# Kernel optimization log

Hardware: AMD Instinct MI355X
Metric: run time of the kernel (lower is better)

Reference implementation:

```python
import jax, jax.numpy as jnp
import numpy as np

B, M, D, H, FF = 2, 2048, 1024, 16, 2624
DH = D // H  # 64, power of 2 as required by the kernel
EPS = 1e-5
THETA = 10000.0


def setup_inputs() -> dict:
    key = jax.random.key(0)
    ks = jax.random.split(key, 12)
    hidden_states = jax.random.normal(ks[0], (B, M, D), dtype=jnp.float32)
    # padding mask: 1=valid, 0=pad; vary valid lengths per batch element
    lengths = jnp.array([M, 3 * M // 4], dtype=jnp.int32)
    attention_mask = (jnp.arange(M)[None, :] < lengths[:, None]).astype(jnp.int32)
    s = 0.02
    return {
        "hidden_states": hidden_states,
        "attention_mask": attention_mask,
        "ln1_w": jnp.ones((D,), jnp.float32),
        "ln1_b": jnp.zeros((D,), jnp.float32),
        "wqkv_w": s * jax.random.normal(ks[1], (3 * D, D), jnp.float32),
        "wqkv_b": jnp.zeros((3 * D,), jnp.float32),
        "wo_w": s * jax.random.normal(ks[2], (D, D), jnp.float32),
        "ln2_w": jnp.ones((D,), jnp.float32),
        "ln2_b": jnp.zeros((D,), jnp.float32),
        "wi_w": s * jax.random.normal(ks[3], (2 * FF, D), jnp.float32),
        "wo_mlp_w": s * jax.random.normal(ks[4], (D, FF), jnp.float32),
    }


def _layernorm(x, w, b):
    mu = jnp.mean(x, axis=-1, keepdims=True)
    var = jnp.mean(jnp.square(x - mu), axis=-1, keepdims=True)
    return (x - mu) * jax.lax.rsqrt(var + EPS) * w + b


def _rope(q, k):
    # q,k: [B,H,M,DH]; half-split RoPE (q1' = q1*c - q2*s; q2' = q1*s + q2*c)
    half = DH // 2
    inv_freq = 1.0 / (THETA ** (jnp.arange(0, DH, 2, dtype=jnp.float32) / DH))  # [half]
    freqs = jnp.arange(M, dtype=jnp.float32)[:, None] * inv_freq[None, :]      # [M, half]
    c = jnp.cos(freqs)[None, None]  # [1,1,M,half]
    s = jnp.sin(freqs)[None, None]
    q1, q2 = q[..., :half], q[..., half:]
    k1, k2 = k[..., :half], k[..., half:]
    q = jnp.concatenate([q1 * c - q2 * s, q1 * s + q2 * c], axis=-1)
    k = jnp.concatenate([k1 * c - k2 * s, k1 * s + k2 * c], axis=-1)
    return q, k


def reference(hidden_states, attention_mask, ln1_w, ln1_b, wqkv_w, wqkv_b,
              wo_w, ln2_w, ln2_b, wi_w, wo_mlp_w):
    x = hidden_states
    xn = _layernorm(x, ln1_w, ln1_b)
    qkv = (xn @ wqkv_w.T + wqkv_b).reshape(B, M, 3, H, DH)
    q, k, v = [jnp.transpose(qkv[:, :, i], (0, 2, 1, 3)) for i in range(3)]  # [B,H,M,DH]
    q, k = _rope(q, k)
    scale = 1.0 / np.sqrt(DH)
    scores = jnp.einsum("bhmd,bhnd->bhmn", q, k) * scale
    keep = (attention_mask > 0)[:, None, None, :]  # [B,1,1,M] key-padding mask
    scores = jnp.where(keep, scores, -jnp.inf)
    attn = jax.nn.softmax(scores, axis=-1)
    o = jnp.einsum("bhmn,bhnd->bhmd", attn, v)
    attn_out = jnp.transpose(o, (0, 2, 1, 3)).reshape(B, M, D)
    x = x + attn_out @ wo_w.T
    # ModernBERT GeGLU MLP
    h = _layernorm(x, ln2_w, ln2_b)
    g = h @ wi_w.T
    inp, gate = g[..., :FF], g[..., FF:]
    x = x + (jax.nn.gelu(inp, approximate=False) * gate) @ wo_mlp_w.T
    return x
```

## Files before the change

kernel.cpp:

```cpp
#include <hip/hip_runtime.h>
#include <hip/hip_bf16.h>
#include <math.h>

#define BB 2
#define MM 2048
#define DD 1024
#define HH 16
#define DHH 64
#define FF_ 2624
#define FFP 2688
#define TT (BB*MM)

typedef unsigned short u16;
typedef __attribute__((ext_vector_type(4))) unsigned short ushort4v;
typedef __attribute__((ext_vector_type(8))) short short8;
typedef __attribute__((ext_vector_type(4))) float floatx4;

#define SCALE2 0.18033688011112043f

__device__ __forceinline__ u16 f2bf(float f) {
    __hip_bfloat16 h = __float2bfloat16(f);
    return *(u16*)&h;
}
__device__ __forceinline__ float bf2f(u16 u) {
    __hip_bfloat16 h; *(u16*)&h = u;
    return __bfloat162float(h);
}
__device__ __forceinline__ float gelu_exact(float x) {
    return 0.5f * x * (1.0f + erff(x * 0.70710678118654752f));
}
__device__ __forceinline__ void gload_lds16(const void* g, void* l) {
    __builtin_amdgcn_global_load_lds(
        (const __attribute__((address_space(1))) unsigned int*)g,
        (__attribute__((address_space(3))) unsigned int*)l, 16, 0, 0);
}

__global__ void cvt_all(const float* __restrict__ wqkv, const float* __restrict__ wo,
                        const float* __restrict__ wi, const float* __restrict__ womlp,
                        u16* __restrict__ dqkv, u16* __restrict__ dwo,
                        u16* __restrict__ dinp, u16* __restrict__ dgate,
                        u16* __restrict__ dmlp) {
    int bid = blockIdx.x, tid = threadIdx.x;
    if (bid < 3072) {
        int i = (bid * 256 + tid) * 4;
        float4 v = *(const float4*)(wqkv + i);
        ushort4v o = {f2bf(v.x), f2bf(v.y), f2bf(v.z), f2bf(v.w)};
        *(ushort4v*)(dqkv + i) = o;
    } else if (bid < 4096) {
        int i = ((bid - 3072) * 256 + tid) * 4;
        float4 v = *(const float4*)(wo + i);
        ushort4v o = {f2bf(v.x), f2bf(v.y), f2bf(v.z), f2bf(v.w)};
        *(ushort4v*)(dwo + i) = o;
    } else if (bid < 4096 + 2 * FFP) {
        int seg = (bid - 4096) / FFP;
        int row = (bid - 4096) % FFP;
        u16* dst = seg ? dgate : dinp;
        const float* src = wi + (size_t)(seg ? FF_ : 0) * DD;
        int c = tid * 4;
        ushort4v o = {0, 0, 0, 0};
        if (row < FF_) {
            float4 v = *(const float4*)(src + (size_t)row * DD + c);
            o.x = f2bf(v.x); o.y = f2bf(v.y); o.z = f2bf(v.z); o.w = f2bf(v.w);
        }
        *(ushort4v*)(dst + (size_t)row * DD + c) = o;
    } else {
        int row = bid - 4096 - 2 * FFP;
        for (int c = tid * 4; c < FFP; c += 1024) {
            ushort4v o = {0, 0, 0, 0};
            if (c < FF_) {
                float4 v = *(const float4*)(womlp + (size_t)row * FF_ + c);
                o.x = f2bf(v.x); o.y = f2bf(v.y); o.z = f2bf(v.z); o.w = f2bf(v.w);
            }
            *(ushort4v*)(dmlp + (size_t)row * FFP + c) = o;
        }
    }
}

__global__ void ln_kernel(const float* __restrict__ x, const float* __restrict__ w,
                          const float* __restrict__ b, u16* __restrict__ out) {
    int row = blockIdx.x;
    int tid = threadIdx.x;
    const float4 v = ((const float4*)(x + (size_t)row * DD))[tid];
    float s  = v.x + v.y + v.z + v.w;
    float ss = v.x*v.x + v.y*v.y + v.z*v.z + v.w*v.w;
    #pragma unroll
    for (int o = 32; o > 0; o >>= 1) { s += __shfl_down(s, o); ss += __shfl_down(ss, o); }
    __shared__ float sbuf[4], ssbuf[4];
    int wid = tid >> 6;
    if ((tid & 63) == 0) { sbuf[wid] = s; ssbuf[wid] = ss; }
    __syncthreads();
    float st  = sbuf[0] + sbuf[1] + sbuf[2] + sbuf[3];
    float sst = ssbuf[0] + ssbuf[1] + ssbuf[2] + ssbuf[3];
    float mean = st * (1.0f / DD);
    float var  = sst * (1.0f / DD) - mean * mean;
    float rstd = rsqrtf(var + 1e-5f);
    const float4 wv = ((const float4*)w)[tid];
    const float4 bv = ((const float4*)b)[tid];
    ushort4v o;
    o.x = f2bf((v.x - mean) * rstd * wv.x + bv.x);
    o.y = f2bf((v.y - mean) * rstd * wv.y + bv.y);
    o.z = f2bf((v.z - mean) * rstd * wv.z + bv.z);
    o.w = f2bf((v.w - mean) * rstd * wv.w + bv.w);
    ((ushort4v*)(out + (size_t)row * DD))[tid] = o;
}

template<int MODE, bool OUT_BF16>
__global__ __launch_bounds__(256)
void mfma_gemm(const u16* __restrict__ A, const u16* __restrict__ W,
               const float* __restrict__ bias, const void* __restrict__ add,
               void* __restrict__ Cout, int N, int K) {
    __shared__ u16 As[128 * 64];
    __shared__ u16 Bs[128 * 64];
    int tid = threadIdx.x;
    int w = tid >> 6, lane = tid & 63;
    int q = lane >> 4, m = lane & 15;
    int row0 = blockIdx.y * 128, col0 = blockIdx.x * 128;
    int wm = (w >> 1) * 64, wn = (w & 1) * 64;

    floatx4 acc[4][4];
    #pragma unroll
    for (int i = 0; i < 4; i++)
        #pragma unroll
        for (int j = 0; j < 4; j++)
            acc[i][j] = (floatx4){0.f, 0.f, 0.f, 0.f};

    int lrow = lane >> 3;
    int lcg  = (lane & 7) ^ lrow;
    const u16* Ag = A + (size_t)(row0 + w * 32 + lrow) * K + lcg * 8;
    const u16* Bg = W + (size_t)(col0 + w * 32 + lrow) * K + lcg * 8;
    u16* Al = &As[(w * 32) * 64];
    u16* Bl = &Bs[(w * 32) * 64];

    for (int kt = 0; kt < K; kt += 64) {
        __syncthreads();
        #pragma unroll
        for (int t = 0; t < 4; t++) {
            gload_lds16(Ag + (size_t)(t * 8) * K, Al + t * 8 * 64);
            gload_lds16(Bg + (size_t)(t * 8) * K, Bl + t * 8 * 64);
        }
        Ag += 64; Bg += 64;
        __syncthreads();
        #pragma unroll
        for (int s = 0; s < 2; s++) {
            short8 af[4], bf[4];
            #pragma unroll
            for (int f = 0; f < 4; f++) {
                int slot = (s * 4 + q) ^ (m & 7);
                af[f] = *(const short8*)&As[(wm + f * 16 + m) * 64 + slot * 8];
                bf[f] = *(const short8*)&Bs[(wn + f * 16 + m) * 64 + slot * 8];
            }
            #pragma unroll
            for (int mf = 0; mf < 4; mf++)
                #pragma unroll
                for (int nf = 0; nf < 4; nf++)
                    acc[mf][nf] = __builtin_amdgcn_mfma_f32_16x16x32_bf16(
                        af[mf], bf[nf], acc[mf][nf], 0, 0, 0);
        }
    }

    #pragma unroll
    for (int nf = 0; nf < 4; nf++) {
        int col = col0 + wn + nf * 16 + m;
        float bv = 0.f;
        if (MODE == 0 && bias) bv = bias[col];
        #pragma unroll
        for (int mf = 0; mf < 4; mf++) {
            #pragma unroll
            for (int r = 0; r < 4; r++) {
                int row = row0 + wm + mf * 16 + q * 4 + r;
                size_t idx = (size_t)row * N + col;
                float vacc = acc[mf][nf][r] + bv;
                if (MODE == 1) vacc += ((const float*)add)[idx];
                if (OUT_BF16) ((u16*)Cout)[idx] = f2bf(vacc);
                else          ((float*)Cout)[idx] = vacc;
            }
        }
    }
}

__global__ __launch_bounds__(256, 2)
void mfma_gemm_glu(const u16* __restrict__ A, const u16* __restrict__ W1,
                   const u16* __restrict__ W2, u16* __restrict__ Cout) {
    __shared__ u16 As[128 * 64];
    __shared__ u16 B1s[128 * 64];
    __shared__ u16 B2s[128 * 64];
    int tid = threadIdx.x;
    int w = tid >> 6, lane = tid & 63;
    int q = lane >> 4, m = lane & 15;
    int row0 = blockIdx.y * 128, col0 = blockIdx.x * 128;
    int wm = (w >> 1) * 64, wn = (w & 1) * 64;

    floatx4 acc1[4][4], acc2[4][4];
    #pragma unroll
    for (int i = 0; i < 4; i++)
        #pragma unroll
        for (int j = 0; j < 4; j++) {
            acc1[i][j] = (floatx4){0.f, 0.f, 0.f, 0.f};
            acc2[i][j] = (floatx4){0.f, 0.f, 0.f, 0.f};
        }

    int lrow = lane >> 3;
    int lcg  = (lane & 7) ^ lrow;
    const u16* Ag  = A  + (size_t)(row0 + w * 32 + lrow) * DD + lcg * 8;
    const u16* B1g = W1 + (size_t)(col0 + w * 32 + lrow) * DD + lcg * 8;
    const u16* B2g = W2 + (size_t)(col0 + w * 32 + lrow) * DD + lcg * 8;
    u16* Al  = &As [(w * 32) * 64];
    u16* B1l = &B1s[(w * 32) * 64];
    u16* B2l = &B2s[(w * 32) * 64];

    for (int kt = 0; kt < DD; kt += 64) {
        __syncthreads();
        #pragma unroll
        for (int t = 0; t < 4; t++) {
            gload_lds16(Ag  + (size_t)(t * 8) * DD, Al  + t * 8 * 64);
            gload_lds16(B1g + (size_t)(t * 8) * DD, B1l + t * 8 * 64);
            gload_lds16(B2g + (size_t)(t * 8) * DD, B2l + t * 8 * 64);
        }
        Ag += 64; B1g += 64; B2g += 64;
        __syncthreads();
        #pragma unroll
        for (int s = 0; s < 2; s++) {
            short8 af[4], b1f[4], b2f[4];
            #pragma unroll
            for (int f = 0; f < 4; f++) {
                int slot = (s * 4 + q) ^ (m & 7);
                af[f]  = *(const short8*)&As [(wm + f * 16 + m) * 64 + slot * 8];
                b1f[f] = *(const short8*)&B1s[(wn + f * 16 + m) * 64 + slot * 8];
                b2f[f] = *(const short8*)&B2s[(wn + f * 16 + m) * 64 + slot * 8];
            }
            #pragma unroll
            for (int mf = 0; mf < 4; mf++)
                #pragma unroll
                for (int nf = 0; nf < 4; nf++) {
                    acc1[mf][nf] = __builtin_amdgcn_mfma_f32_16x16x32_bf16(
                        af[mf], b1f[nf], acc1[mf][nf], 0, 0, 0);
                    acc2[mf][nf] = __builtin_amdgcn_mfma_f32_16x16x32_bf16(
                        af[mf], b2f[nf], acc2[mf][nf], 0, 0, 0);
                }
        }
    }

    #pragma unroll
    for (int nf = 0; nf < 4; nf++) {
        int col = col0 + wn + nf * 16 + m;
        #pragma unroll
        for (int mf = 0; mf < 4; mf++) {
            #pragma unroll
            for (int r = 0; r < 4; r++) {
                int row = row0 + wm + mf * 16 + q * 4 + r;
                Cout[(size_t)row * FFP + col] =
                    f2bf(gelu_exact(acc1[mf][nf][r]) * acc2[mf][nf][r]);
            }
        }
    }
}

__global__ void rope_qk(const u16* __restrict__ qkv, u16* __restrict__ q,
                        u16* __restrict__ k) {
    int t = blockIdx.x;
    int h = blockIdx.y;
    int b = t >> 11, mi = t & 2047;
    int lane = threadIdx.x;
    int i = lane & 31;
    const u16* base = qkv + (size_t)t * (3 * DD) + h * DHH + (lane < 32 ? 0 : DD);
    u16* dst = (lane < 32 ? q : k) + (((size_t)(b * HH + h)) * MM + mi) * DHH;
    float x1 = bf2f(base[i]);
    float x2 = bf2f(base[i + 32]);
    float inv_freq = powf(10000.0f, -2.0f * (float)i / 64.0f);
    float fr = (float)mi * inv_freq;
    float c = cosf(fr), s = sinf(fr);
    dst[i]      = f2bf(x1 * c - x2 * s);
    dst[i + 32] = f2bf(x1 * s + x2 * c);
}

__global__ void vt_trans(const u16* __restrict__ qkv, u16* __restrict__ vt) {
    __shared__ u16 Ls[64][72];
    int m0 = blockIdx.x * 64, h = blockIdx.y, b = blockIdx.z;
    int tid = threadIdx.x;
    const u16* src = qkv + ((size_t)(b * MM + m0)) * (3 * DD) + 2 * DD + h * DHH;
    #pragma unroll
    for (int u = 0; u < 2; u++) {
        int r = (tid >> 3) + u * 32, c8 = tid & 7;
        *(short8*)&Ls[r][c8 * 8] = *(const short8*)(src + (size_t)r * (3 * DD) + c8 * 8);
    }
    __syncthreads();
    u16* dst = vt + ((size_t)(b * HH + h)) * DHH * MM;
    #pragma unroll
    for (int u = 0; u < 2; u++) {
        int d = (tid >> 3) + u * 32, c8 = tid & 7;
        short8 o;
        #pragma unroll
        for (int j = 0; j < 8; j++) o[j] = (short)Ls[c8 * 8 + j][d];
        *(short8*)(dst + (size_t)d * MM + m0 + c8 * 8) = o;
    }
}

__global__ __launch_bounds__(256, 2)
void flash_attn_mfma(const u16* __restrict__ q, const u16* __restrict__ k,
                     const u16* __restrict__ vt, const int* __restrict__ mask,
                     u16* __restrict__ out) {
    __shared__ __align__(16) u16 Ks[64 * 64];
    __shared__ __align__(16) u16 Vt[64 * 64];
    __shared__ __align__(16) u16 QP[128 * 64];

    int tid = threadIdx.x;
    int w = tid >> 6, lane = tid & 63;
    int quad = lane >> 4, m = lane & 15;
    int mt = blockIdx.x, h = blockIdx.y, b = blockIdx.z;
    int m0 = mt * 128;
    size_t bh = (size_t)(b * HH + h);
    const u16* qb  = q  + (bh * MM + m0) * DHH;
    const u16* kb  = k  + bh * MM * DHH;
    const u16* vtb = vt + bh * DHH * MM;

    int lrow = lane >> 3, lcg = (lane & 7) ^ lrow;

    {
        const u16* Qg = qb + (size_t)(w * 32 + lrow) * DHH + lcg * 8;
        u16* Ql = &QP[(w * 32) * 64];
        #pragma unroll
        for (int t = 0; t < 4; t++)
            gload_lds16(Qg + (size_t)(t * 8) * DHH, Ql + t * 8 * 64);
    }
    __syncthreads();

    short8 qf[2][2];
    #pragma unroll
    for (int mf = 0; mf < 2; mf++)
        #pragma unroll
        for (int ks = 0; ks < 2; ks++) {
            int slot = (ks * 4 + quad) ^ (m & 7);
            qf[mf][ks] = *(const short8*)&QP[(w * 32 + mf * 16 + m) * 64 + slot * 8];
        }

    floatx4 O[2][4];
    #pragma unroll
    for (int mf = 0; mf < 2; mf++)
        #pragma unroll
        for (int df = 0; df < 4; df++)
            O[mf][df] = (floatx4){0.f, 0.f, 0.f, 0.f};
    float lsum[2][4] = {};

    u16* Pw = &QP[(w * 32) * 64];

    for (int n0 = 0; n0 < MM; n0 += 64) {
        if (mask[b * MM + n0] == 0) break;
        __syncthreads();

        {
            const u16* Kg = kb + (size_t)(n0 + w * 16 + lrow) * DHH + lcg * 8;
            u16* Kl = &Ks[(w * 16) * 64];
            #pragma unroll
            for (int t = 0; t < 2; t++)
                gload_lds16(Kg + (size_t)(t * 8) * DHH, Kl + t * 8 * 64);
            const u16* Vg = vtb + (size_t)(w * 16 + lrow) * MM + n0 + lcg * 8;
            u16* Vl = &Vt[(w * 16) * 64];
            #pragma unroll
            for (int t = 0; t < 2; t++)
                gload_lds16(Vg + (size_t)(t * 8) * MM, Vl + t * 8 * 64);
        }
        __syncthreads();

        floatx4 S[2][4];
        #pragma unroll
        for (int mf = 0; mf < 2; mf++)
            #pragma unroll
            for (int nf = 0; nf < 4; nf++)
                S[mf][nf] = (floatx4){0.f, 0.f, 0.f, 0.f};
        #pragma unroll
        for (int ks = 0; ks < 2; ks++) {
            short8 kf[4];
            #pragma unroll
            for (int nf = 0; nf < 4; nf++) {
                int slot = (ks * 4 + quad) ^ (m & 7);
                kf[nf] = *(const short8*)&Ks[(nf * 16 + m) * 64 + slot * 8];
            }
            #pragma unroll
            for (int mf = 0; mf < 2; mf++)
                #pragma unroll
                for (int nf = 0; nf < 4; nf++)
                    S[mf][nf] = __builtin_amdgcn_mfma_f32_16x16x32_bf16(
                        qf[mf][ks], kf[nf], S[mf][nf], 0, 0, 0);
        }

        #pragma unroll
        for (int mf = 0; mf < 2; mf++)
            #pragma unroll
            for (int r = 0; r < 4; r++) {
                float s0 = exp2f(S[mf][0][r] * SCALE2);
                float s1 = exp2f(S[mf][1][r] * SCALE2);
                float s2 = exp2f(S[mf][2][r] * SCALE2);
                float s3 = exp2f(S[mf][3][r] * SCALE2);
                S[mf][0][r] = s0; S[mf][1][r] = s1; S[mf][2][r] = s2; S[mf][3][r] = s3;
                lsum[mf][r] += (s0 + s1) + (s2 + s3);
            }

        #pragma unroll
        for (int mf = 0; mf < 2; mf++)
            #pragma unroll
            for (int nf = 0; nf < 4; nf++)
                #pragma unroll
                for (int r = 0; r < 4; r++) {
                    int prow = mf * 16 + quad * 4 + r;
                    int pcol = nf * 16 + m;
                    int slot = (pcol >> 3) ^ (prow & 7);
                    Pw[prow * 64 + slot * 8 + (pcol & 7)] = f2bf(S[mf][nf][r]);
                }

        #pragma unroll
        for (int ks = 0; ks < 2; ks++) {
            short8 pf[2], vf[4];
            #pragma unroll
            for (int mf = 0; mf < 2; mf++) {
                int slot = (ks * 4 + quad) ^ (m & 7);
                pf[mf] = *(const short8*)&Pw[(mf * 16 + m) * 64 + slot * 8];
            }
            #pragma unroll
            for (int df = 0; df < 4; df++) {
                int d = df * 16 + m;
                int slot = (ks * 4 + quad) ^ (d & 7);
                vf[df] = *(const short8*)&Vt[d * 64 + slot * 8];
            }
            #pragma unroll
            for (int mf = 0; mf < 2; mf++)
                #pragma unroll
                for (int df = 0; df < 4; df++)
                    O[mf][df] = __builtin_amdgcn_mfma_f32_16x16x32_bf16(
                        pf[mf], vf[df], O[mf][df], 0, 0, 0);
        }
    }

    #pragma unroll
    for (int mf = 0; mf < 2; mf++) {
        float inv[4];
        #pragma unroll
        for (int r = 0; r < 4; r++) {
            float s = lsum[mf][r];
            #pragma unroll
            for (int o = 1; o < 16; o <<= 1) s += __shfl_xor(s, o);
            inv[r] = 1.0f / s;
        }
        #pragma unroll
        for (int df = 0; df < 4; df++) {
            int d = df * 16 + m;
            #pragma unroll
            for (int r = 0; r < 4; r++) {
                int row = m0 + w * 32 + mf * 16 + quad * 4 + r;
                out[((size_t)(b * MM) + row) * DD + h * DHH + d] =
                    f2bf(O[mf][df][r] * inv[r]);
            }
        }
    }
}

extern "C" void kernel_launch(void* const* d_in, const int* in_sizes, int n_in,
                              void* d_out, int out_size, void* d_ws, size_t ws_size,
                              hipStream_t stream) {
    const float* hidden   = (const float*)d_in[0];
    const int*   mask     = (const int*)d_in[1];
    const float* ln1_w    = (const float*)d_in[2];
    const float* ln1_b    = (const float*)d_in[3];
    const float* wqkv_w   = (const float*)d_in[4];
    const float* wqkv_b   = (const float*)d_in[5];
    const float* wo_w     = (const float*)d_in[6];
    const float* ln2_w    = (const float*)d_in[7];
    const float* ln2_b    = (const float*)d_in[8];
    const float* wi_w     = (const float*)d_in[9];
    const float* wo_mlp_w = (const float*)d_in[10];
    float* out = (float*)d_out;

    char* ws = (char*)d_ws;
    u16* wqkv_bf  = (u16*)(ws);
    u16* wo_bf    = (u16*)(ws + 6291456);
    u16* wi_inp   = (u16*)(ws + 8388608);
    u16* wi_gate  = (u16*)(ws + 13893632);
    u16* womlp_bf = (u16*)(ws + 19398656);
    u16* xn       = (u16*)(ws + 24903680);
    u16* qkv      = (u16*)(ws + 33292288);
    u16* qb       = (u16*)(ws + 58458112);
    u16* kb       = (u16*)(ws + 66846720);
    u16* vtb      = (u16*)(ws + 75235328);
    u16* attn_out = (u16*)(ws + 83623936);
    u16* hb       = (u16*)(ws + 92012544);
    u16* act      = (u16*)(ws + 58458112);

    cvt_all<<<4096 + 2 * FFP + 1024, 256, 0, stream>>>(
        wqkv_w, wo_w, wi_w, wo_mlp_w, wqkv_bf, wo_bf, wi_inp, wi_gate, womlp_bf);
    ln_kernel<<<TT, 256, 0, stream>>>(hidden, ln1_w, ln1_b, xn);
    mfma_gemm<0, true><<<dim3(3 * DD / 128, TT / 128), 256, 0, stream>>>(
        xn, wqkv_bf, wqkv_b, nullptr, qkv, 3 * DD, DD);
    rope_qk<<<dim3(TT, HH), 64, 0, stream>>>(qkv, qb, kb);
    vt_trans<<<dim3(MM / 64, HH, BB), 256, 0, stream>>>(qkv, vtb);
    flash_attn_mfma<<<dim3(MM / 128, HH, BB), 256, 0, stream>>>(qb, kb, vtb, mask, attn_out);
    mfma_gemm<1, false><<<dim3(DD / 128, TT / 128), 256, 0, stream>>>(
        attn_out, wo_bf, nullptr, hidden, out, DD, DD);
    ln_kernel<<<TT, 256, 0, stream>>>(out, ln2_w, ln2_b, hb);
    mfma_gemm_glu<<<dim3(FFP / 128, TT / 128), 256, 0, stream>>>(
        hb, wi_inp, wi_gate, act);
    mfma_gemm<1, false><<<dim3(DD / 128, TT / 128), 256, 0, stream>>>(
        act, womlp_bf, nullptr, out, out, DD, FFP);
}
```

Baseline: 398.9 us.

## Fuse RoPE and V transpose into QKV GEMM epilogue; double-buffer GEMM K-loop

The QKV projection GEMM now applies RoPE and writes q/k in head-major layout and V transposed directly from its epilogue. This removes the intermediate qkv buffer and the separate rope_qk and vt_trans kernels. A cos/sin table is precomputed in the weight-conversion kernel. All GEMMs switch to a double-buffered 32-wide K loop with one barrier per step, MFMA priority raising, and an XCD-aware block swizzle. These changes add more barriers per unit of K and scattered epilogue stores in exchange for fewer launches and less memory traffic.

```diff
diff --git a/kernel.cpp b/kernel.cpp
--- a/kernel.cpp
+++ b/kernel.cpp
@@ -35,11 +35,16 @@
         (__attribute__((address_space(3))) unsigned int*)l, 16, 0, 0);
 }
 
+__device__ __forceinline__ int xcd_swizzle(int id, int nb) {
+    if (nb & 7) return id;
+    return (id & 7) * (nb >> 3) + (id >> 3);
+}
+
 __global__ void cvt_all(const float* __restrict__ wqkv, const float* __restrict__ wo,
                         const float* __restrict__ wi, const float* __restrict__ womlp,
                         u16* __restrict__ dqkv, u16* __restrict__ dwo,
                         u16* __restrict__ dinp, u16* __restrict__ dgate,
-                        u16* __restrict__ dmlp) {
+                        u16* __restrict__ dmlp, float2* __restrict__ tab) {
     int bid = blockIdx.x, tid = threadIdx.x;
     if (bid < 3072) {
         int i = (bid * 256 + tid) * 4;
@@ -63,7 +68,7 @@
             o.x = f2bf(v.x); o.y = f2bf(v.y); o.z = f2bf(v.z); o.w = f2bf(v.w);
         }
         *(ushort4v*)(dst + (size_t)row * DD + c) = o;
-    } else {
+    } else if (bid < 4096 + 2 * FFP + 1024) {
         int row = bid - 4096 - 2 * FFP;
         for (int c = tid * 4; c < FFP; c += 1024) {
             ushort4v o = {0, 0, 0, 0};
@@ -72,6 +77,15 @@
                 o.x = f2bf(v.x); o.y = f2bf(v.y); o.z = f2bf(v.z); o.w = f2bf(v.w);
             }
             *(ushort4v*)(dmlp + (size_t)row * FFP + c) = o;
+        }
+    } else {
+        int bq = bid - (4096 + 2 * FFP + 1024);
+        int base = bq * 1024;
+        for (int idx = tid; idx < 1024; idx += 256) {
+            int e = base + idx;
+            int mi = e >> 5, i = e & 31;
+            float fr = (float)mi * powf(10000.0f, -(float)i / 32.0f);
+            tab[e] = make_float2(cosf(fr), sinf(fr));
         }
     }
 }
@@ -104,17 +118,22 @@
     ((ushort4v*)(out + (size_t)row * DD))[tid] = o;
 }
 
+
 template<int MODE, bool OUT_BF16>
 __global__ __launch_bounds__(256)
 void mfma_gemm(const u16* __restrict__ A, const u16* __restrict__ W,
                const float* __restrict__ bias, const void* __restrict__ add,
                void* __restrict__ Cout, int N, int K) {
-    __shared__ u16 As[128 * 64];
-    __shared__ u16 Bs[128 * 64];
+    __shared__ u16 As[2][128 * 32];
+    __shared__ u16 Bs[2][128 * 32];
     int tid = threadIdx.x;
     int w = tid >> 6, lane = tid & 63;
     int q = lane >> 4, m = lane & 15;
-    int row0 = blockIdx.y * 128, col0 = blockIdx.x * 128;
+
+    int nbx = gridDim.x;
+    int id = xcd_swizzle(blockIdx.y * nbx + blockIdx.x, nbx * gridDim.y);
+    int bx = id % nbx, by = id / nbx;
+    int row0 = by * 128, col0 = bx * 128;
     int wm = (w >> 1) * 64, wn = (w & 1) * 64;
 
     floatx4 acc[4][4];
@@ -124,38 +143,44 @@
         for (int j = 0; j < 4; j++)
             acc[i][j] = (floatx4){0.f, 0.f, 0.f, 0.f};
 
-    int lrow = lane >> 3;
-    int lcg  = (lane & 7) ^ lrow;
+    int lrow = lane >> 2;
+    int lcg  = (lane & 3) ^ ((lrow >> 1) & 3);
     const u16* Ag = A + (size_t)(row0 + w * 32 + lrow) * K + lcg * 8;
     const u16* Bg = W + (size_t)(col0 + w * 32 + lrow) * K + lcg * 8;
-    u16* Al = &As[(w * 32) * 64];
-    u16* Bl = &Bs[(w * 32) * 64];
-
-    for (int kt = 0; kt < K; kt += 64) {
-        __syncthreads();
-        #pragma unroll
-        for (int t = 0; t < 4; t++) {
-            gload_lds16(Ag + (size_t)(t * 8) * K, Al + t * 8 * 64);
-            gload_lds16(Bg + (size_t)(t * 8) * K, Bl + t * 8 * 64);
-        }
-        Ag += 64; Bg += 64;
-        __syncthreads();
-        #pragma unroll
-        for (int s = 0; s < 2; s++) {
-            short8 af[4], bf[4];
-            #pragma unroll
-            for (int f = 0; f < 4; f++) {
-                int slot = (s * 4 + q) ^ (m & 7);
-                af[f] = *(const short8*)&As[(wm + f * 16 + m) * 64 + slot * 8];
-                bf[f] = *(const short8*)&Bs[(wn + f * 16 + m) * 64 + slot * 8];
-            }
-            #pragma unroll
-            for (int mf = 0; mf < 4; mf++)
-                #pragma unroll
-                for (int nf = 0; nf < 4; nf++)
-                    acc[mf][nf] = __builtin_amdgcn_mfma_f32_16x16x32_bf16(
-                        af[mf], bf[nf], acc[mf][nf], 0, 0, 0);
-        }
+    int NT = K >> 5;
+    int slot8 = (q ^ ((m >> 1) & 3)) * 8;
+
+    gload_lds16(Ag,                    &As[0][(w * 32) * 32]);
+    gload_lds16(Ag + (size_t)16 * K,   &As[0][(w * 32 + 16) * 32]);
+    gload_lds16(Bg,                    &Bs[0][(w * 32) * 32]);
+    gload_lds16(Bg + (size_t)16 * K,   &Bs[0][(w * 32 + 16) * 32]);
+    __syncthreads();
+
+    for (int t = 0; t < NT; ++t) {
+        int cur = t & 1;
+        if (t + 1 < NT) {
+            const u16* Aq = Ag + (size_t)(t + 1) * 32;
+            const u16* Bq = Bg + (size_t)(t + 1) * 32;
+            gload_lds16(Aq,                  &As[cur ^ 1][(w * 32) * 32]);
+            gload_lds16(Aq + (size_t)16 * K, &As[cur ^ 1][(w * 32 + 16) * 32]);
+            gload_lds16(Bq,                  &Bs[cur ^ 1][(w * 32) * 32]);
+            gload_lds16(Bq + (size_t)16 * K, &Bs[cur ^ 1][(w * 32 + 16) * 32]);
+        }
+        short8 af[4], bf[4];
+        #pragma unroll
+        for (int f = 0; f < 4; f++) {
+            af[f] = *(const short8*)&As[cur][(wm + f * 16 + m) * 32 + slot8];
+            bf[f] = *(const short8*)&Bs[cur][(wn + f * 16 + m) * 32 + slot8];
+        }
+        __builtin_amdgcn_s_setprio(1);
+        #pragma unroll
+        for (int mf = 0; mf < 4; mf++)
+            #pragma unroll
+            for (int nf = 0; nf < 4; nf++)
+                acc[mf][nf] = __builtin_amdgcn_mfma_f32_16x16x32_bf16(
+                    af[mf], bf[nf], acc[mf][nf], 0, 0, 0);
+        __builtin_amdgcn_s_setprio(0);
+        if (t + 1 < NT) __syncthreads();
     }
 
     #pragma unroll
@@ -178,16 +203,133 @@
     }
 }
 
+__global__ __launch_bounds__(256)
+void mfma_gemm_qkv(const u16* __restrict__ A, const u16* __restrict__ W,
+                   const float* __restrict__ bias, const float2* __restrict__ tab,
+                   u16* __restrict__ qb, u16* __restrict__ kb, u16* __restrict__ vtb) {
+    __shared__ u16 As[2][128 * 32];
+    __shared__ u16 Bs[2][128 * 32];
+    int tid = threadIdx.x;
+    int w = tid >> 6, lane = tid & 63;
+    int q = lane >> 4, m = lane & 15;
+
+    int nbx = gridDim.x;
+    int id = xcd_swizzle(blockIdx.y * nbx + blockIdx.x, nbx * gridDim.y);
+    int bx = id % nbx, by = id / nbx;
+    int row0 = by * 128, col0 = bx * 128;
+    int wm = (w >> 1) * 64, wn = (w & 1) * 64;
+
+    floatx4 acc[4][4];
+    #pragma unroll
+    for (int i = 0; i < 4; i++)
+        #pragma unroll
+        for (int j = 0; j < 4; j++)
+            acc[i][j] = (floatx4){0.f, 0.f, 0.f, 0.f};
+
+    int lrow = lane >> 2;
+    int lcg  = (lane & 3) ^ ((lrow >> 1) & 3);
+    const u16* Ag = A + (size_t)(row0 + w * 32 + lrow) * DD + lcg * 8;
+    const u16* Bg = W + (size_t)(col0 + w * 32 + lrow) * DD + lcg * 8;
+    const int NT = DD >> 5;
+    int slot8 = (q ^ ((m >> 1) & 3)) * 8;
+
+    gload_lds16(Ag,                     &As[0][(w * 32) * 32]);
+    gload_lds16(Ag + (size_t)16 * DD,   &As[0][(w * 32 + 16) * 32]);
+    gload_lds16(Bg,                     &Bs[0][(w * 32) * 32]);
+    gload_lds16(Bg + (size_t)16 * DD,   &Bs[0][(w * 32 + 16) * 32]);
+    __syncthreads();
+
+    for (int t = 0; t < NT; ++t) {
+        int cur = t & 1;
+        if (t + 1 < NT) {
+            const u16* Aq = Ag + (size_t)(t + 1) * 32;
+            const u16* Bq = Bg + (size_t)(t + 1) * 32;
+            gload_lds16(Aq,                   &As[cur ^ 1][(w * 32) * 32]);
+            gload_lds16(Aq + (size_t)16 * DD, &As[cur ^ 1][(w * 32 + 16) * 32]);
+            gload_lds16(Bq,                   &Bs[cur ^ 1][(w * 32) * 32]);
+            gload_lds16(Bq + (size_t)16 * DD, &Bs[cur ^ 1][(w * 32 + 16) * 32]);
+        }
+        short8 af[4], bf[4];
+        #pragma unroll
+        for (int f = 0; f < 4; f++) {
+            af[f] = *(const short8*)&As[cur][(wm + f * 16 + m) * 32 + slot8];
+            bf[f] = *(const short8*)&Bs[cur][(wn + f * 16 + m) * 32 + slot8];
+        }
+        __builtin_amdgcn_s_setprio(1);
+        #pragma unroll
+        for (int mf = 0; mf < 4; mf++)
+            #pragma unroll
+            for (int nf = 0; nf < 4; nf++)
+                acc[mf][nf] = __builtin_amdgcn_mfma_f32_16x16x32_bf16(
+                    af[mf], bf[nf], acc[mf][nf], 0, 0, 0);
+        __builtin_amdgcn_s_setprio(0);
+        if (t + 1 < NT) __syncthreads();
+    }
+
+    int wcol = col0 + wn;
+    int seg  = wcol >> 6;
+    int b    = row0 >> 11;
+    int mi0  = (row0 & 2047) + wm;
+
+    float b0[4];
+    #pragma unroll
+    for (int nf = 0; nf < 4; nf++) b0[nf] = bias[wcol + nf * 16 + m];
+
+    if (seg < 32) {
+        int hq = seg & 15;
+        u16* dst = (seg < 16 ? qb : kb) + (size_t)(b * HH + hq) * MM * DHH;
+        #pragma unroll
+        for (int mf = 0; mf < 4; mf++) {
+            #pragma unroll
+            for (int r = 0; r < 4; r++) {
+                int mi = mi0 + mf * 16 + q * 4 + r;
+                float2 cs0 = tab[mi * 32 + m];
+                float2 cs1 = tab[mi * 32 + 16 + m];
+                float a0 = acc[mf][0][r] + b0[0];
+                float a1 = acc[mf][1][r] + b0[1];
+                float a2 = acc[mf][2][r] + b0[2];
+                float a3 = acc[mf][3][r] + b0[3];
+                size_t base = (size_t)mi * DHH;
+                dst[base + m]      = f2bf(a0 * cs0.x - a2 * cs0.y);
+                dst[base + 32 + m] = f2bf(a0 * cs0.y + a2 * cs0.x);
+                dst[base + 16 + m] = f2bf(a1 * cs1.x - a3 * cs1.y);
+                dst[base + 48 + m] = f2bf(a1 * cs1.y + a3 * cs1.x);
+            }
+        }
+    } else {
+        int hv = seg & 15;
+        u16* dst = vtb + (size_t)(b * HH + hv) * DHH * MM;
+        #pragma unroll
+        for (int nf = 0; nf < 4; nf++) {
+            int d = nf * 16 + m;
+            #pragma unroll
+            for (int mf = 0; mf < 4; mf++) {
+                int mi = mi0 + mf * 16 + q * 4;
+                ushort4v o;
+                o.x = f2bf(acc[mf][nf][0] + b0[nf]);
+                o.y = f2bf(acc[mf][nf][1] + b0[nf]);
+                o.z = f2bf(acc[mf][nf][2] + b0[nf]);
+                o.w = f2bf(acc[mf][nf][3] + b0[nf]);
+                *(ushort4v*)(dst + (size_t)d * MM + mi) = o;
+            }
+        }
+    }
+}
+
 __global__ __launch_bounds__(256, 2)
 void mfma_gemm_glu(const u16* __restrict__ A, const u16* __restrict__ W1,
                    const u16* __restrict__ W2, u16* __restrict__ Cout) {
-    __shared__ u16 As[128 * 64];
-    __shared__ u16 B1s[128 * 64];
-    __shared__ u16 B2s[128 * 64];
+    __shared__ u16 As [2][128 * 32];
+    __shared__ u16 B1s[2][128 * 32];
+    __shared__ u16 B2s[2][128 * 32];
     int tid = threadIdx.x;
     int w = tid >> 6, lane = tid & 63;
     int q = lane >> 4, m = lane & 15;
-    int row0 = blockIdx.y * 128, col0 = blockIdx.x * 128;
+
+    int nbx = gridDim.x;
+    int id = xcd_swizzle(blockIdx.y * nbx + blockIdx.x, nbx * gridDim.y);
+    int bx = id % nbx, by = id / nbx;
+    int row0 = by * 128, col0 = bx * 128;
     int wm = (w >> 1) * 64, wn = (w & 1) * 64;
 
     floatx4 acc1[4][4], acc2[4][4];
@@ -199,45 +341,54 @@
             acc2[i][j] = (floatx4){0.f, 0.f, 0.f, 0.f};
         }
 
-    int lrow = lane >> 3;
-    int lcg  = (lane & 7) ^ lrow;
+    int lrow = lane >> 2;
+    int lcg  = (lane & 3) ^ ((lrow >> 1) & 3);
     const u16* Ag  = A  + (size_t)(row0 + w * 32 + lrow) * DD + lcg * 8;
     const u16* B1g = W1 + (size_t)(col0 + w * 32 + lrow) * DD + lcg * 8;
     const u16* B2g = W2 + (size_t)(col0 + w * 32 + lrow) * DD + lcg * 8;
-    u16* Al  = &As [(w * 32) * 64];
-    u16* B1l = &B1s[(w * 32) * 64];
-    u16* B2l = &B2s[(w * 32) * 64];
-
-    for (int kt = 0; kt < DD; kt += 64) {
-        __syncthreads();
-        #pragma unroll
-        for (int t = 0; t < 4; t++) {
-            gload_lds16(Ag  + (size_t)(t * 8) * DD, Al  + t * 8 * 64);
-            gload_lds16(B1g + (size_t)(t * 8) * DD, B1l + t * 8 * 64);
-            gload_lds16(B2g + (size_t)(t * 8) * DD, B2l + t * 8 * 64);
-        }
-        Ag += 64; B1g += 64; B2g += 64;
-        __syncthreads();
-        #pragma unroll
-        for (int s = 0; s < 2; s++) {
-            short8 af[4], b1f[4], b2f[4];
-            #pragma unroll
-            for (int f = 0; f < 4; f++) {
-                int slot = (s * 4 + q) ^ (m & 7);
-                af[f]  = *(const short8*)&As [(wm + f * 16 + m) * 64 + slot * 8];
-                b1f[f] = *(const short8*)&B1s[(wn + f * 16 + m) * 64 + slot * 8];
-                b2f[f] = *(const short8*)&B2s[(wn + f * 16 + m) * 64 + slot * 8];
-            }
-            #pragma unroll
-            for (int mf = 0; mf < 4; mf++)
-                #pragma unroll
-                for (int nf = 0; nf < 4; nf++) {
-                    acc1[mf][nf] = __builtin_amdgcn_mfma_f32_16x16x32_bf16(
-                        af[mf], b1f[nf], acc1[mf][nf], 0, 0, 0);
-                    acc2[mf][nf] = __builtin_amdgcn_mfma_f32_16x16x32_bf16(
-                        af[mf], b2f[nf], acc2[mf][nf], 0, 0, 0);
-                }
-        }
+    const int NT = DD >> 5;
+    int slot8 = (q ^ ((m >> 1) & 3)) * 8;
+
+    gload_lds16(Ag,                    &As [0][(w * 32) * 32]);
+    gload_lds16(Ag  + (size_t)16 * DD, &As [0][(w * 32 + 16) * 32]);
+    gload_lds16(B1g,                   &B1s[0][(w * 32) * 32]);
+    gload_lds16(B1g + (size_t)16 * DD, &B1s[0][(w * 32 + 16) * 32]);
+    gload_lds16(B2g,                   &B2s[0][(w * 32) * 32]);
+    gload_lds16(B2g + (size_t)16 * DD, &B2s[0][(w * 32 + 16) * 32]);
+    __syncthreads();
+
+    for (int t = 0; t < NT; ++t) {
+        int cur = t & 1;
+        if (t + 1 < NT) {
+            const u16* Aq  = Ag  + (size_t)(t + 1) * 32;
+            const u16* B1q = B1g + (size_t)(t + 1) * 32;
+            const u16* B2q = B2g + (size_t)(t + 1) * 32;
+            gload_lds16(Aq,                    &As [cur ^ 1][(w * 32) * 32]);
+            gload_lds16(Aq  + (size_t)16 * DD, &As [cur ^ 1][(w * 32 + 16) * 32]);
+            gload_lds16(B1q,                   &B1s[cur ^ 1][(w * 32) * 32]);
+            gload_lds16(B1q + (size_t)16 * DD, &B1s[cur ^ 1][(w * 32 + 16) * 32]);
+            gload_lds16(B2q,                   &B2s[cur ^ 1][(w * 32) * 32]);
+            gload_lds16(B2q + (size_t)16 * DD, &B2s[cur ^ 1][(w * 32 + 16) * 32]);
+        }
+        short8 af[4], b1f[4], b2f[4];
+        #pragma unroll
+        for (int f = 0; f < 4; f++) {
+            af[f]  = *(const short8*)&As [cur][(wm + f * 16 + m) * 32 + slot8];
+            b1f[f] = *(const short8*)&B1s[cur][(wn + f * 16 + m) * 32 + slot8];
+            b2f[f] = *(const short8*)&B2s[cur][(wn + f * 16 + m) * 32 + slot8];
+        }
+        __builtin_amdgcn_s_setprio(1);
+        #pragma unroll
+        for (int mf = 0; mf < 4; mf++)
+            #pragma unroll
+            for (int nf = 0; nf < 4; nf++) {
+                acc1[mf][nf] = __builtin_amdgcn_mfma_f32_16x16x32_bf16(
+                    af[mf], b1f[nf], acc1[mf][nf], 0, 0, 0);
+                acc2[mf][nf] = __builtin_amdgcn_mfma_f32_16x16x32_bf16(
+                    af[mf], b2f[nf], acc2[mf][nf], 0, 0, 0);
+            }
+        __builtin_amdgcn_s_setprio(0);
+        if (t + 1 < NT) __syncthreads();
     }
 
     #pragma unroll
@@ -252,46 +403,6 @@
                     f2bf(gelu_exact(acc1[mf][nf][r]) * acc2[mf][nf][r]);
             }
         }
-    }
-}
-
-__global__ void rope_qk(const u16* __restrict__ qkv, u16* __restrict__ q,
-                        u16* __restrict__ k) {
-    int t = blockIdx.x;
-    int h = blockIdx.y;
-    int b = t >> 11, mi = t & 2047;
-    int lane = threadIdx.x;
-    int i = lane & 31;
-    const u16* base = qkv + (size_t)t * (3 * DD) + h * DHH + (lane < 32 ? 0 : DD);
-    u16* dst = (lane < 32 ? q : k) + (((size_t)(b * HH + h)) * MM + mi) * DHH;
-    float x1 = bf2f(base[i]);
-    float x2 = bf2f(base[i + 32]);
-    float inv_freq = powf(10000.0f, -2.0f * (float)i / 64.0f);
-    float fr = (float)mi * inv_freq;
-    float c = cosf(fr), s = sinf(fr);
-    dst[i]      = f2bf(x1 * c - x2 * s);
-    dst[i + 32] = f2bf(x1 * s + x2 * c);
-}
-
-__global__ void vt_trans(const u16* __restrict__ qkv, u16* __restrict__ vt) {
-    __shared__ u16 Ls[64][72];
-    int m0 = blockIdx.x * 64, h = blockIdx.y, b = blockIdx.z;
-    int tid = threadIdx.x;
-    const u16* src = qkv + ((size_t)(b * MM + m0)) * (3 * DD) + 2 * DD + h * DHH;
-    #pragma unroll
-    for (int u = 0; u < 2; u++) {
-        int r = (tid >> 3) + u * 32, c8 = tid & 7;
-        *(short8*)&Ls[r][c8 * 8] = *(const short8*)(src + (size_t)r * (3 * DD) + c8 * 8);
-    }
-    __syncthreads();
-    u16* dst = vt + ((size_t)(b * HH + h)) * DHH * MM;
-    #pragma unroll
-    for (int u = 0; u < 2; u++) {
-        int d = (tid >> 3) + u * 32, c8 = tid & 7;
-        short8 o;
-        #pragma unroll
-        for (int j = 0; j < 8; j++) o[j] = (short)Ls[c8 * 8 + j][d];
-        *(short8*)(dst + (size_t)d * MM + m0 + c8 * 8) = o;
     }
 }
 
@@ -476,7 +587,7 @@
     u16* wi_gate  = (u16*)(ws + 13893632);
     u16* womlp_bf = (u16*)(ws + 19398656);
     u16* xn       = (u16*)(ws + 24903680);
-    u16* qkv      = (u16*)(ws + 33292288);
+    float2* rtab  = (float2*)(ws + 33292288);
     u16* qb       = (u16*)(ws + 58458112);
     u16* kb       = (u16*)(ws + 66846720);
     u16* vtb      = (u16*)(ws + 75235328);
@@ -484,13 +595,11 @@
     u16* hb       = (u16*)(ws + 92012544);
     u16* act      = (u16*)(ws + 58458112);
 
-    cvt_all<<<4096 + 2 * FFP + 1024, 256, 0, stream>>>(
-        wqkv_w, wo_w, wi_w, wo_mlp_w, wqkv_bf, wo_bf, wi_inp, wi_gate, womlp_bf);
+    cvt_all<<<4096 + 2 * FFP + 1024 + 64, 256, 0, stream>>>(
+        wqkv_w, wo_w, wi_w, wo_mlp_w, wqkv_bf, wo_bf, wi_inp, wi_gate, womlp_bf, rtab);
     ln_kernel<<<TT, 256, 0, stream>>>(hidden, ln1_w, ln1_b, xn);
-    mfma_gemm<0, true><<<dim3(3 * DD / 128, TT / 128), 256, 0, stream>>>(
-        xn, wqkv_bf, wqkv_b, nullptr, qkv, 3 * DD, DD);
-    rope_qk<<<dim3(TT, HH), 64, 0, stream>>>(qkv, qb, kb);
-    vt_trans<<<dim3(MM / 64, HH, BB), 256, 0, stream>>>(qkv, vtb);
+    mfma_gemm_qkv<<<dim3(3 * DD / 128, TT / 128), 256, 0, stream>>>(
+        xn, wqkv_bf, wqkv_b, rtab, qb, kb, vtb);
     flash_attn_mfma<<<dim3(MM / 128, HH, BB), 256, 0, stream>>>(qb, kb, vtb, mask, attn_out);
     mfma_gemm<1, false><<<dim3(DD / 128, TT / 128), 256, 0, stream>>>(
         attn_out, wo_bf, nullptr, hidden, out, DD, DD);
```

Result: slower. 411.6 us (+3.2%).
